# Performance work log

Measured on AMD Instinct MI355X. Metric: run time of the kernel, lower is better.

Reference implementation:

```python
import jax, jax.numpy as jnp
import numpy as np

IN_DIM = 128
OUT_DIM = 128
H = 8
HD = OUT_DIM // H  # 16
EPS = 1e-5
NEG = -1e30


def setup_inputs() -> dict:
    key = jax.random.key(0)
    ks = jax.random.split(key, 10)
    B, N = 8, 1024
    h = jax.random.normal(ks[0], (B, N, IN_DIM), dtype=jnp.float32)
    adj_mask = jax.random.randint(ks[1], (B, N, N), 0, 2, dtype=jnp.int32)
    s = 1.0 / np.sqrt(IN_DIM)
    W = jax.random.normal(ks[2], (H, IN_DIM, HD), dtype=jnp.float32) * s
    a = jax.random.normal(ks[3], (H, 2 * HD), dtype=jnp.float32) * (1.0 / np.sqrt(2 * HD))
    ln1_g = jnp.ones((OUT_DIM,), jnp.float32)
    ln1_b = jnp.zeros((OUT_DIM,), jnp.float32)
    w1 = jax.random.normal(ks[4], (OUT_DIM, 2 * OUT_DIM), dtype=jnp.float32) * (1.0 / np.sqrt(OUT_DIM))
    b1 = jnp.zeros((2 * OUT_DIM,), jnp.float32)
    w2 = jax.random.normal(ks[5], (2 * OUT_DIM, OUT_DIM), dtype=jnp.float32) * (1.0 / np.sqrt(2 * OUT_DIM))
    b2 = jnp.zeros((OUT_DIM,), jnp.float32)
    ln2_g = jnp.ones((OUT_DIM,), jnp.float32)
    ln2_b = jnp.zeros((OUT_DIM,), jnp.float32)
    return dict(h=h, adj_mask=adj_mask, W=W, a=a, ln1_g=ln1_g, ln1_b=ln1_b,
                w1=w1, b1=b1, w2=w2, b2=b2, ln2_g=ln2_g, ln2_b=ln2_b)


def _layernorm(x, g, b):
    mu = jnp.mean(x, axis=-1, keepdims=True)
    var = jnp.mean(jnp.square(x - mu), axis=-1, keepdims=True)
    return (x - mu) * jax.lax.rsqrt(var + EPS) * g + b


def reference(h, adj_mask, W, a, ln1_g, ln1_b, w1, b1, w2, b2, ln2_g, ln2_b):
    B, N, _ = h.shape
    # Per-head projection: (B,H,N,HD)
    Wh = jnp.einsum('bni,hid->bhnd', h, W)
    # a.[Wh_i, Wh_j] = a_src.Wh_i + a_dst.Wh_j (decompose concat-score)
    a_src, a_dst = a[:, :HD], a[:, HD:]
    s_i = jnp.einsum('bhnd,hd->bhn', Wh, a_src)  # source term
    s_j = jnp.einsum('bhnd,hd->bhn', Wh, a_dst)  # target term
    e = s_i[:, :, :, None] + s_j[:, :, None, :]  # (B,H,N,N)
    e = jnp.where(e >= 0, e, 0.2 * e)            # LeakyReLU(0.2)
    mask = (adj_mask != 0)[:, None, :, :]        # (B,1,N,N)
    e = jnp.where(mask, e, NEG)
    alpha = jax.nn.softmax(e, axis=-1)
    # rows with no neighbors -> NaN in torch softmax -> zeroed; replicate
    row_valid = jnp.any(mask, axis=-1, keepdims=True)  # (B,1,N,1)
    alpha = jnp.where(row_valid, alpha, 0.0)
    # dropout in eval mode = identity
    h_heads = jnp.einsum('bhnm,bhmd->bhnd', alpha, Wh)
    h_cat = h_heads.transpose(0, 2, 1, 3).reshape(B, N, H * HD)
    # residual (in_dim == out_dim here)
    h_cat = _layernorm(h_cat + h, ln1_g, ln1_b)
    ffn = jnp.maximum(h_cat @ w1 + b1, 0.0) @ w2 + b2
    return _layernorm(h_cat + ffn, ln2_g, ln2_b)
```

## Files before the change

kernel.cpp:

```cpp
#include <hip/hip_runtime.h>
#include <hip/hip_bf16.h>

#define IN_DIM 128
#define OUT_DIM 128
#define NHEAD 8
#define HD 16
#define BB 8
#define NN 1024
#define LOG2E 1.44269504f

typedef unsigned long long u64;
typedef float f32x4 __attribute__((ext_vector_type(4)));
typedef short bf16x8 __attribute__((ext_vector_type(8)));


__global__ __launch_bounds__(256) void k_pack(const int* __restrict__ adj,
                                              unsigned* __restrict__ bits_t,
                                              const float* __restrict__ w1,
                                              const float* __restrict__ w2,
                                              unsigned short* __restrict__ w1T,
                                              unsigned short* __restrict__ w2T) {
    __shared__ float tile[32][33];
    int t = threadIdx.x;
    if (blockIdx.x < 2048) {
        int lane = t & 63;
        int wave_id = blockIdx.x * 4 + (t >> 6);
        int b = wave_id >> 10, i = wave_id & 1023;
        const int4* rowp = (const int4*)(adj + ((size_t)(b * 1024 + i)) * 1024);
        int4 v0 = rowp[lane];
        int4 v1 = rowp[64 + lane];
        int4 v2 = rowp[128 + lane];
        int4 v3 = rowp[192 + lane];
        u64 B0x = __ballot(v0.x != 0), B0y = __ballot(v0.y != 0), B0z = __ballot(v0.z != 0), B0w = __ballot(v0.w != 0);
        u64 B1x = __ballot(v1.x != 0), B1y = __ballot(v1.y != 0), B1z = __ballot(v1.z != 0), B1w = __ballot(v1.w != 0);
        u64 B2x = __ballot(v2.x != 0), B2y = __ballot(v2.y != 0), B2z = __ballot(v2.z != 0), B2w = __ballot(v2.w != 0);
        u64 B3x = __ballot(v3.x != 0), B3y = __ballot(v3.y != 0), B3z = __ballot(v3.z != 0), B3w = __ballot(v3.w != 0);
        if (lane == 0) {
            unsigned* dst = bits_t + (size_t)b * 32 * 1024 + i;
#define STW(ch, c, B) \
            dst[((ch) * 8 + (c) * 2 + 0) * 1024] = (unsigned)(B); \
            dst[((ch) * 8 + (c) * 2 + 1) * 1024] = (unsigned)((B) >> 32);
            STW(0, 0, B0x) STW(0, 1, B0y) STW(0, 2, B0z) STW(0, 3, B0w)
            STW(1, 0, B1x) STW(1, 1, B1y) STW(1, 2, B1z) STW(1, 3, B1w)
            STW(2, 0, B2x) STW(2, 1, B2y) STW(2, 2, B2z) STW(2, 3, B2w)
            STW(3, 0, B3x) STW(3, 1, B3y) STW(3, 2, B3z) STW(3, 3, B3w)
#undef STW
        }
    } else {
        int blk = blockIdx.x - 2048;
        const float* src; unsigned short* dst; int R, C;
        if (blk < 32) { src = w1; dst = w1T; R = 128; C = 256; }
        else          { src = w2; dst = w2T; R = 256; C = 128; blk -= 32; }
        int tpr = C >> 5;
        int tr = blk / tpr, tc = blk - tr * tpr;
        int r0 = tr << 5, c0 = tc << 5;
        int lr = t >> 5, lc = t & 31;
#pragma unroll
        for (int p = 0; p < 4; ++p)
            tile[lr + p * 8][lc] = src[(size_t)(r0 + lr + p * 8) * C + c0 + lc];
        __syncthreads();
#pragma unroll
        for (int p = 0; p < 4; ++p) {
            __hip_bfloat16 bv = __float2bfloat16(tile[lc][lr + p * 8]);
            dst[(size_t)(c0 + lr + p * 8) * R + r0 + lc] = *(unsigned short*)&bv;
        }
    }
}

__global__ __launch_bounds__(256) void k_wh(
    const float* __restrict__ hin, const float* __restrict__ W,
    const float* __restrict__ a,
    unsigned short* __restrict__ whT, float* __restrict__ si_g,
    float* __restrict__ sj_g)
{
    extern __shared__ float smem[];
    float* h_s  = smem;
    float* wt_s = smem + 32 * 132;
    int t = threadIdx.x;
    int blk = blockIdx.x;
    int b = blk >> 5;
    int ntile = blk & 31;
    const float* hrow = hin + ((size_t)b * NN + ntile * 32) * IN_DIM;

#pragma unroll
    for (int it = 0; it < 4; ++it) {
        int g = t + 256 * it;
        int row = g >> 5, c4 = g & 31;
        float4 v = ((const float4*)hrow)[g];
        *(float4*)&h_s[row * 132 + c4 * 4] = v;
    }
    for (int g = t; g < (NHEAD * IN_DIM * HD) / 4; g += 256) {
        int hh = g >> 9;
        int rem = g & 511;
        int i = rem >> 2, d4 = rem & 3;
        float4 v = ((const float4*)W)[g];
        wt_s[(hh * 16 + d4 * 4 + 0) * 132 + i] = v.x;
        wt_s[(hh * 16 + d4 * 4 + 1) * 132 + i] = v.y;
        wt_s[(hh * 16 + d4 * 4 + 2) * 132 + i] = v.z;
        wt_s[(hh * 16 + d4 * 4 + 3) * 132 + i] = v.w;
    }
    __syncthreads();

    int d4 = t & 3;
    int hq = (t >> 2) & 7;
    int ngrp = t >> 5;
    float acc[4][4];
#pragma unroll
    for (int q = 0; q < 4; ++q)
#pragma unroll
        for (int dd = 0; dd < 4; ++dd) acc[q][dd] = 0.f;

    for (int i4 = 0; i4 < 32; ++i4) {
        float4 wr[4], hv[4];
#pragma unroll
        for (int dd = 0; dd < 4; ++dd)
            wr[dd] = *(const float4*)&wt_s[(hq * 16 + d4 * 4 + dd) * 132 + i4 * 4];
#pragma unroll
        for (int q = 0; q < 4; ++q)
            hv[q] = *(const float4*)&h_s[(ngrp * 4 + q) * 132 + i4 * 4];
#pragma unroll
        for (int q = 0; q < 4; ++q)
#pragma unroll
            for (int dd = 0; dd < 4; ++dd)
                acc[q][dd] += hv[q].x * wr[dd].x + hv[q].y * wr[dd].y +
                              hv[q].z * wr[dd].z + hv[q].w * wr[dd].w;
    }

    int bh = b * NHEAD + hq;
    int rowbase = ntile * 32 + ngrp * 4;
    int p0 = ((rowbase >> 8) << 8) | ((rowbase >> 2) & 63);

    float asrc[4], adst[4];
#pragma unroll
    for (int dd = 0; dd < 4; ++dd) {
        asrc[dd] = a[hq * 32 + d4 * 4 + dd];
        adst[dd] = a[hq * 32 + 16 + d4 * 4 + dd];
    }
#pragma unroll
    for (int q = 0; q < 4; ++q) {
        float psi = acc[q][0] * asrc[0] + acc[q][1] * asrc[1] + acc[q][2] * asrc[2] + acc[q][3] * asrc[3];
        float psj = acc[q][0] * adst[0] + acc[q][1] * adst[1] + acc[q][2] * adst[2] + acc[q][3] * adst[3];
        psi += __shfl_xor(psi, 1); psi += __shfl_xor(psi, 2);
        psj += __shfl_xor(psj, 1); psj += __shfl_xor(psj, 2);
        if (d4 == 0) {
            si_g[(size_t)bh * NN + rowbase + q] = psi * LOG2E;
            sj_g[(size_t)bh * NN + p0 + q * 64] = psj * LOG2E;
        }
    }

#pragma unroll
    for (int dd = 0; dd < 4; ++dd) {
        unsigned u0, u1;
        asm("v_cvt_pk_bf16_f32 %0, %1, %2" : "=v"(u0) : "v"(acc[0][dd]), "v"(acc[1][dd]));
        asm("v_cvt_pk_bf16_f32 %0, %1, %2" : "=v"(u1) : "v"(acc[2][dd]), "v"(acc[3][dd]));
        size_t basei = (size_t)(bh * 16 + d4 * 4 + dd) * 1024 + p0;
        whT[basei]       = (unsigned short)(u0 & 0xffff);
        whT[basei + 64]  = (unsigned short)(u0 >> 16);
        whT[basei + 128] = (unsigned short)(u1 & 0xffff);
        whT[basei + 192] = (unsigned short)(u1 >> 16);
    }
}

__global__ __launch_bounds__(512, 3) void k_attn(
    const unsigned short* __restrict__ whT,
    const unsigned* __restrict__ bits_t,
    const float* __restrict__ si_g, const float* __restrict__ sj_g,
    float* __restrict__ hh)
{
    __shared__ __align__(16) unsigned short whT_s[16 * 1032];
    __shared__ __align__(16) float ejp_s[NN];
    __shared__ __align__(16) float ejn_s[NN];
    int t = threadIdx.x;
    int blk = blockIdx.x;
    int part = blk & 7;
    int bh = blk >> 3;
    int hq = bh & 7, b = bh >> 3;
    int blkrow = part * 128;

    {
        const uint4* src = (const uint4*)(whT + (size_t)bh * 16 * 1024);
#pragma unroll
        for (int it = 0; it < 4; ++it) {
            int g = t + 512 * it;
            int d = g >> 7, c8 = g & 127;
            uint4 v = src[g];
            *(uint4*)&whT_s[d * 1032 + c8 * 8] = v;
        }
#pragma unroll
        for (int jt = 0; jt < 2; ++jt) {
            int j = t + jt * 512;
            float sjv = sj_g[(size_t)bh * NN + j];
            float ep, en;
            asm("v_exp_f32 %0, %1" : "=v"(ep) : "v"(sjv));
            asm("v_exp_f32 %0, %1" : "=v"(en) : "v"(0.2f * sjv));
            ejp_s[j] = ep;
            ejn_s[j] = en;
        }
    }
    __syncthreads();

    int wv = t >> 6, lane = t & 63;
    int lo16 = lane & 15, g = lane >> 4;
    int row = blkrow + wv * 16 + lo16;
    float siL = si_g[(size_t)bh * NN + row];
    float esip, esin;
    asm("v_exp_f32 %0, %1" : "=v"(esip) : "v"(siL));
    asm("v_exp_f32 %0, %1" : "=v"(esin) : "v"(0.2f * siL));
    const unsigned* mcol = bits_t + (size_t)b * 32 * 1024 + row;

    const unsigned short* wbase = &whT_s[lo16 * 1032 + g * 8];
    const float* pbase = &ejp_s[g * 8];
    const float* nbase = &ejn_s[g * 8];

    f32x4 acc = {0.f, 0.f, 0.f, 0.f};
    float lsA = 0.f, lsB = 0.f;
    unsigned m = mcol[0];
#pragma unroll 4
    for (int kt = 0; kt < 32; ++kt) {
        unsigned m_next = (kt < 31) ? mcol[(size_t)(kt + 1) * 1024] : 0u;
        bf16x8 bfrag = *(const bf16x8*)&wbase[kt * 32];
        float4 pa = *(const float4*)&pbase[kt * 32];
        float4 pb = *(const float4*)&pbase[kt * 32 + 4];
        float4 na = *(const float4*)&nbase[kt * 32];
        float4 nb = *(const float4*)&nbase[kt * 32 + 4];
        unsigned mm = m >> (g * 8);
        float q0 = fmaxf(esip * pa.x, esin * na.x); q0 = (mm & 1u)   ? q0 : 0.f;
        float q1 = fmaxf(esip * pa.y, esin * na.y); q1 = (mm & 2u)   ? q1 : 0.f;
        float q2 = fmaxf(esip * pa.z, esin * na.z); q2 = (mm & 4u)   ? q2 : 0.f;
        float q3 = fmaxf(esip * pa.w, esin * na.w); q3 = (mm & 8u)   ? q3 : 0.f;
        float q4 = fmaxf(esip * pb.x, esin * nb.x); q4 = (mm & 16u)  ? q4 : 0.f;
        float q5 = fmaxf(esip * pb.y, esin * nb.y); q5 = (mm & 32u)  ? q5 : 0.f;
        float q6 = fmaxf(esip * pb.z, esin * nb.z); q6 = (mm & 64u)  ? q6 : 0.f;
        float q7 = fmaxf(esip * pb.w, esin * nb.w); q7 = (mm & 128u) ? q7 : 0.f;
        lsA += (q0 + q2) + (q4 + q6);
        lsB += (q1 + q3) + (q5 + q7);
        union { bf16x8 v; __hip_bfloat16 h[8]; } af;
        af.h[0] = __float2bfloat16(q0);
        af.h[1] = __float2bfloat16(q1);
        af.h[2] = __float2bfloat16(q2);
        af.h[3] = __float2bfloat16(q3);
        af.h[4] = __float2bfloat16(q4);
        af.h[5] = __float2bfloat16(q5);
        af.h[6] = __float2bfloat16(q6);
        af.h[7] = __float2bfloat16(q7);
        acc = __builtin_amdgcn_mfma_f32_16x16x32_bf16(af.v, bfrag, acc, 0, 0, 0);
        m = m_next;
    }

    float lsum = lsA + lsB;
    lsum += __shfl_xor(lsum, 16);
    lsum += __shfl_xor(lsum, 32);

    float* obase = hh + ((size_t)b * NN + blkrow + wv * 16) * OUT_DIM + hq * HD + lo16;
#pragma unroll
    for (int q = 0; q < 4; ++q) {
        float ls = __shfl(lsum, 4 * g + q);
        float r = (ls > 0.f) ? 1.0f / ls : 0.f;
        obase[(size_t)(4 * g + q) * OUT_DIM] = acc[q] * r;
    }
}

__global__ __launch_bounds__(512, 1) void k_ffn(const float* __restrict__ hhs,
                                                const float* __restrict__ hin,
                                                const float* __restrict__ g1,
                                                const float* __restrict__ bt1,
                                                const unsigned short* __restrict__ w1T,
                                                const float* __restrict__ bb1,
                                                const unsigned short* __restrict__ w2T,
                                                const float* __restrict__ bb2,
                                                const float* __restrict__ g2,
                                                const float* __restrict__ bt2,
                                                float* __restrict__ out) {
    __shared__ float xc_f[32][128];
    __shared__ float y_f[32][132];
    __shared__ __align__(16) unsigned short xc_bf[32 * 128];
    __shared__ __align__(16) unsigned short hid_bf[32 * 256];

    int t = threadIdx.x;
    int R0 = blockIdx.x * 32;
    int wv = t >> 6, lane = t & 63;
    int lo = lane & 15, g = lane >> 4;

    bf16x8 b1f[2][4];
#pragma unroll
    for (int jt = 0; jt < 2; ++jt) {
        int n = (wv * 2 + jt) * 16 + lo;
#pragma unroll
        for (int kt = 0; kt < 4; ++kt)
            b1f[jt][kt] = *(const bf16x8*)&w1T[(size_t)n * 128 + kt * 32 + g * 8];
    }
    bf16x8 b2f[8];
    {
        int n = wv * 16 + lo;
#pragma unroll
        for (int kt = 0; kt < 8; ++kt)
            b2f[kt] = *(const bf16x8*)&w2T[(size_t)n * 256 + kt * 32 + g * 8];
    }
    float b1v[2];
    b1v[0] = bb1[(wv * 2 + 0) * 16 + lo];
    b1v[1] = bb1[(wv * 2 + 1) * 16 + lo];
    float b2v = bb2[wv * 16 + lo];

    {
        int r = t >> 4, c = t & 15;
        size_t row = (size_t)(R0 + r) * 128;
        float4 ha = *(const float4*)&hhs[row + c * 8];
        float4 hb = *(const float4*)&hhs[row + c * 8 + 4];
        float4 ia = *(const float4*)&hin[row + c * 8];
        float4 ib = *(const float4*)&hin[row + c * 8 + 4];
        float x[8] = {ha.x + ia.x, ha.y + ia.y, ha.z + ia.z, ha.w + ia.w,
                      hb.x + ib.x, hb.y + ib.y, hb.z + ib.z, hb.w + ib.w};
        float s = 0.f, s2 = 0.f;
#pragma unroll
        for (int j = 0; j < 8; ++j) { s += x[j]; s2 += x[j] * x[j]; }
#pragma unroll
        for (int off = 8; off > 0; off >>= 1) {
            s += __shfl_xor(s, off);
            s2 += __shfl_xor(s2, off);
        }
        float mu = s * (1.f / 128.f);
        float var = s2 * (1.f / 128.f) - mu * mu;
        float rs = rsqrtf(var + 1e-5f);
        float4 ga = *(const float4*)&g1[c * 8], gb = *(const float4*)&g1[c * 8 + 4];
        float4 ba = *(const float4*)&bt1[c * 8], bb = *(const float4*)&bt1[c * 8 + 4];
        float gg[8] = {ga.x, ga.y, ga.z, ga.w, gb.x, gb.y, gb.z, gb.w};
        float bbv[8] = {ba.x, ba.y, ba.z, ba.w, bb.x, bb.y, bb.z, bb.w};
        float xo[8];
#pragma unroll
        for (int j = 0; j < 8; ++j) xo[j] = (x[j] - mu) * rs * gg[j] + bbv[j];
        *(float4*)&xc_f[r][c * 8]     = make_float4(xo[0], xo[1], xo[2], xo[3]);
        *(float4*)&xc_f[r][c * 8 + 4] = make_float4(xo[4], xo[5], xo[6], xo[7]);
        union { uint4 v; unsigned u[4]; } pk;
#pragma unroll
        for (int q = 0; q < 4; ++q)
            asm("v_cvt_pk_bf16_f32 %0, %1, %2" : "=v"(pk.u[q]) : "v"(xo[2 * q]), "v"(xo[2 * q + 1]));
        int byte = (r * 256 + c * 16) ^ ((r & 7) << 4);
        *(uint4*)((char*)xc_bf + byte) = pk.v;
    }
    __syncthreads();

    {
        bf16x8 af[2][4];
#pragma unroll
        for (int mt = 0; mt < 2; ++mt) {
            int m = mt * 16 + lo;
#pragma unroll
            for (int kt = 0; kt < 4; ++kt) {
                int byte = (m * 256 + kt * 64 + g * 16) ^ ((m & 7) << 4);
                af[mt][kt] = *(const bf16x8*)((const char*)xc_bf + byte);
            }
        }
#pragma unroll
        for (int mt = 0; mt < 2; ++mt)
#pragma unroll
            for (int jt = 0; jt < 2; ++jt) {
                f32x4 acc = {0.f, 0.f, 0.f, 0.f};
#pragma unroll
                for (int kt = 0; kt < 4; ++kt)
                    acc = __builtin_amdgcn_mfma_f32_16x16x32_bf16(af[mt][kt], b1f[jt][kt], acc, 0, 0, 0);
                int n = (wv * 2 + jt) * 16 + lo;
#pragma unroll
                for (int q = 0; q < 4; ++q) {
                    float hv = fmaxf(acc[q] + b1v[jt], 0.f);
                    int m = mt * 16 + 4 * g + q;
                    int byte = (m * 512 + n * 2) ^ ((m & 7) << 4);
                    __hip_bfloat16 bv = __float2bfloat16(hv);
                    *(unsigned short*)((char*)hid_bf + byte) = *(unsigned short*)&bv;
                }
            }
    }
    __syncthreads();

    {
        f32x4 acc2[2] = {{0.f, 0.f, 0.f, 0.f}, {0.f, 0.f, 0.f, 0.f}};
#pragma unroll
        for (int mt = 0; mt < 2; ++mt) {
            int m = mt * 16 + lo;
#pragma unroll
            for (int kt = 0; kt < 8; ++kt) {
                int byte = (m * 512 + kt * 64 + g * 16) ^ ((m & 7) << 4);
                bf16x8 a = *(const bf16x8*)((const char*)hid_bf + byte);
                acc2[mt] = __builtin_amdgcn_mfma_f32_16x16x32_bf16(a, b2f[kt], acc2[mt], 0, 0, 0);
            }
        }
        int n = wv * 16 + lo;
#pragma unroll
        for (int mt = 0; mt < 2; ++mt)
#pragma unroll
            for (int q = 0; q < 4; ++q)
                y_f[mt * 16 + 4 * g + q][n] = acc2[mt][q] + b2v;
    }
    __syncthreads();

    {
        int r = t >> 4, c = t & 15;
        float xv[8];
        float s = 0.f, s2 = 0.f;
#pragma unroll
        for (int j = 0; j < 8; ++j) {
            float v = xc_f[r][c * 8 + j] + y_f[r][c * 8 + j];
            xv[j] = v; s += v; s2 += v * v;
        }
#pragma unroll
        for (int off = 8; off > 0; off >>= 1) {
            s += __shfl_xor(s, off);
            s2 += __shfl_xor(s2, off);
        }
        float mu = s * (1.f / 128.f);
        float var = s2 * (1.f / 128.f) - mu * mu;
        float rs = rsqrtf(var + 1e-5f);
        float4 ga = *(const float4*)&g2[c * 8], gb = *(const float4*)&g2[c * 8 + 4];
        float4 ba = *(const float4*)&bt2[c * 8], bb = *(const float4*)&bt2[c * 8 + 4];
        float o[8] = {(xv[0] - mu) * rs * ga.x + ba.x, (xv[1] - mu) * rs * ga.y + ba.y,
                      (xv[2] - mu) * rs * ga.z + ba.z, (xv[3] - mu) * rs * ga.w + ba.w,
                      (xv[4] - mu) * rs * gb.x + bb.x, (xv[5] - mu) * rs * gb.y + bb.y,
                      (xv[6] - mu) * rs * gb.z + bb.z, (xv[7] - mu) * rs * gb.w + bb.w};
        size_t row = (size_t)(R0 + r) * 128;
        *(float4*)&out[row + c * 8]     = make_float4(o[0], o[1], o[2], o[3]);
        *(float4*)&out[row + c * 8 + 4] = make_float4(o[4], o[5], o[6], o[7]);
    }
}

extern "C" void kernel_launch(void* const* d_in, const int* in_sizes, int n_in,
                              void* d_out, int out_size, void* d_ws, size_t ws_size,
                              hipStream_t stream) {
    const float* hin  = (const float*)d_in[0];
    const int*   adj  = (const int*)d_in[1];
    const float* W    = (const float*)d_in[2];
    const float* a    = (const float*)d_in[3];
    const float* ln1g = (const float*)d_in[4];
    const float* ln1b = (const float*)d_in[5];
    const float* w1   = (const float*)d_in[6];
    const float* b1   = (const float*)d_in[7];
    const float* w2   = (const float*)d_in[8];
    const float* b2   = (const float*)d_in[9];
    const float* ln2g = (const float*)d_in[10];
    const float* ln2b = (const float*)d_in[11];
    float* out = (float*)d_out;

    unsigned* bits_t    = (unsigned*)d_ws;
    unsigned short* whT = (unsigned short*)((char*)d_ws + (1u << 20));
    float* si_g         = (float*)((char*)d_ws + (3u << 20));
    float* sj_g         = (float*)((char*)d_ws + (3u << 20) + (256u << 10));
    float* hh           = (float*)((char*)d_ws + (3u << 20) + (512u << 10));
    unsigned short* w1T = (unsigned short*)((char*)d_ws + (7u << 20) + (512u << 10));
    unsigned short* w2T = (unsigned short*)((char*)d_ws + (7u << 20) + (512u << 10) + 65536);

    k_pack<<<2112, 256, 0, stream>>>(adj, bits_t, w1, w2, w1T, w2T);
    k_wh<<<BB * 32, 256, (32 * 132 + 128 * 132) * sizeof(float), stream>>>(hin, W, a, whT, si_g, sj_g);
    k_attn<<<BB * NHEAD * 8, 512, 0, stream>>>(whT, bits_t, si_g, sj_g, hh);
    k_ffn<<<BB * NN / 32, 512, 0, stream>>>(hh, hin, ln1g, ln1b, w1T, b1, w2T, b2, ln2g, ln2b, out);
}
```

Before: 56.39 us.

## Fuse all four stages into one cooperative persistent kernel with grid syncs

Replaces the four separate launches (mask packing, projection, attention, FFN) with a single cooperative kernel of 256 blocks that run each stage in turn, separated by grid-wide syncs. Work is redistributed to fit the fixed grid: each block now handles 256 attention rows over two passes and packs four mask rows per wave. The aim is to remove launch gaps and per-kernel tail effects. In exchange, parallelism is capped at one 512-thread block per CU-sized slot, and grid.sync adds its own barrier cost.

New measurement: 217.2 us. 3.85x slower.

```diff
diff --git a/kernel.cpp b/kernel.cpp
--- a/kernel.cpp
+++ b/kernel.cpp
@@ -1,5 +1,8 @@
 #include <hip/hip_runtime.h>
+#include <hip/hip_cooperative_groups.h>
 #include <hip/hip_bf16.h>
+
+namespace cg = cooperative_groups;
 
 #define IN_DIM 128
 #define OUT_DIM 128
@@ -14,410 +17,403 @@
 typedef short bf16x8 __attribute__((ext_vector_type(8)));
 
 
-__global__ __launch_bounds__(256) void k_pack(const int* __restrict__ adj,
-                                              unsigned* __restrict__ bits_t,
-                                              const float* __restrict__ w1,
-                                              const float* __restrict__ w2,
-                                              unsigned short* __restrict__ w1T,
-                                              unsigned short* __restrict__ w2T) {
-    __shared__ float tile[32][33];
+__global__ __launch_bounds__(512, 1) void k_fused(
+    const float* __restrict__ hin, const int* __restrict__ adj,
+    const float* __restrict__ W, const float* __restrict__ a,
+    const float* __restrict__ g1, const float* __restrict__ bt1,
+    const float* __restrict__ w1, const float* __restrict__ b1v_,
+    const float* __restrict__ w2, const float* __restrict__ b2v_,
+    const float* __restrict__ g2, const float* __restrict__ bt2,
+    unsigned* __restrict__ bits_t, unsigned short* __restrict__ whT,
+    float* __restrict__ si_g, float* __restrict__ sj_g,
+    float* __restrict__ hh, unsigned short* __restrict__ w1T,
+    unsigned short* __restrict__ w2T, float* __restrict__ out)
+{
+    __shared__ __align__(16) char smem_raw[84480];
     int t = threadIdx.x;
-    if (blockIdx.x < 2048) {
+    int blk = blockIdx.x;
+    cg::grid_group grid = cg::this_grid();
+
+    {
         int lane = t & 63;
-        int wave_id = blockIdx.x * 4 + (t >> 6);
-        int b = wave_id >> 10, i = wave_id & 1023;
-        const int4* rowp = (const int4*)(adj + ((size_t)(b * 1024 + i)) * 1024);
-        int4 v0 = rowp[lane];
-        int4 v1 = rowp[64 + lane];
-        int4 v2 = rowp[128 + lane];
-        int4 v3 = rowp[192 + lane];
-        u64 B0x = __ballot(v0.x != 0), B0y = __ballot(v0.y != 0), B0z = __ballot(v0.z != 0), B0w = __ballot(v0.w != 0);
-        u64 B1x = __ballot(v1.x != 0), B1y = __ballot(v1.y != 0), B1z = __ballot(v1.z != 0), B1w = __ballot(v1.w != 0);
-        u64 B2x = __ballot(v2.x != 0), B2y = __ballot(v2.y != 0), B2z = __ballot(v2.z != 0), B2w = __ballot(v2.w != 0);
-        u64 B3x = __ballot(v3.x != 0), B3y = __ballot(v3.y != 0), B3z = __ballot(v3.z != 0), B3w = __ballot(v3.w != 0);
-        if (lane == 0) {
-            unsigned* dst = bits_t + (size_t)b * 32 * 1024 + i;
+        int wave_id = blk * 8 + (t >> 6);
+#pragma unroll 1
+        for (int u = 0; u < 4; ++u) {
+            int r = wave_id + u * 2048;
+            int b = r >> 10, i = r & 1023;
+            const int4* rowp = (const int4*)(adj + ((size_t)(b * 1024 + i)) * 1024);
+            int4 v0 = rowp[lane];
+            int4 v1 = rowp[64 + lane];
+            int4 v2 = rowp[128 + lane];
+            int4 v3 = rowp[192 + lane];
+            u64 B0x = __ballot(v0.x != 0), B0y = __ballot(v0.y != 0), B0z = __ballot(v0.z != 0), B0w = __ballot(v0.w != 0);
+            u64 B1x = __ballot(v1.x != 0), B1y = __ballot(v1.y != 0), B1z = __ballot(v1.z != 0), B1w = __ballot(v1.w != 0);
+            u64 B2x = __ballot(v2.x != 0), B2y = __ballot(v2.y != 0), B2z = __ballot(v2.z != 0), B2w = __ballot(v2.w != 0);
+            u64 B3x = __ballot(v3.x != 0), B3y = __ballot(v3.y != 0), B3z = __ballot(v3.z != 0), B3w = __ballot(v3.w != 0);
+            if (lane == 0) {
+                unsigned* dst = bits_t + (size_t)b * 32 * 1024 + i;
 #define STW(ch, c, B) \
-            dst[((ch) * 8 + (c) * 2 + 0) * 1024] = (unsigned)(B); \
-            dst[((ch) * 8 + (c) * 2 + 1) * 1024] = (unsigned)((B) >> 32);
-            STW(0, 0, B0x) STW(0, 1, B0y) STW(0, 2, B0z) STW(0, 3, B0w)
-            STW(1, 0, B1x) STW(1, 1, B1y) STW(1, 2, B1z) STW(1, 3, B1w)
-            STW(2, 0, B2x) STW(2, 1, B2y) STW(2, 2, B2z) STW(2, 3, B2w)
-            STW(3, 0, B3x) STW(3, 1, B3y) STW(3, 2, B3z) STW(3, 3, B3w)
+                dst[((ch) * 8 + (c) * 2 + 0) * 1024] = (unsigned)(B); \
+                dst[((ch) * 8 + (c) * 2 + 1) * 1024] = (unsigned)((B) >> 32);
+                STW(0, 0, B0x) STW(0, 1, B0y) STW(0, 2, B0z) STW(0, 3, B0w)
+                STW(1, 0, B1x) STW(1, 1, B1y) STW(1, 2, B1z) STW(1, 3, B1w)
+                STW(2, 0, B2x) STW(2, 1, B2y) STW(2, 2, B2z) STW(2, 3, B2w)
+                STW(3, 0, B3x) STW(3, 1, B3y) STW(3, 2, B3z) STW(3, 3, B3w)
 #undef STW
-        }
-    } else {
-        int blk = blockIdx.x - 2048;
+            }
+        }
+    }
+    {
+        float* h_s  = (float*)smem_raw;
+        float* wt_s = h_s + 32 * 132;
+        int b = blk >> 5, ntile = blk & 31;
+        const float* hrow = hin + ((size_t)b * NN + ntile * 32) * IN_DIM;
+        for (int g4 = t; g4 < 1024; g4 += 512) {
+            int row = g4 >> 5, c4 = g4 & 31;
+            float4 v = ((const float4*)hrow)[g4];
+            *(float4*)&h_s[row * 132 + c4 * 4] = v;
+        }
+        for (int g4 = t; g4 < (NHEAD * IN_DIM * HD) / 4; g4 += 512) {
+            int hh_ = g4 >> 9;
+            int rem = g4 & 511;
+            int i = rem >> 2, d4 = rem & 3;
+            float4 v = ((const float4*)W)[g4];
+            wt_s[(hh_ * 16 + d4 * 4 + 0) * 132 + i] = v.x;
+            wt_s[(hh_ * 16 + d4 * 4 + 1) * 132 + i] = v.y;
+            wt_s[(hh_ * 16 + d4 * 4 + 2) * 132 + i] = v.z;
+            wt_s[(hh_ * 16 + d4 * 4 + 3) * 132 + i] = v.w;
+        }
+        __syncthreads();
+
+        if (t < 256) {
+            int d4 = t & 3;
+            int hq = (t >> 2) & 7;
+            int ngrp = t >> 5;
+            float acc[4][4];
+#pragma unroll
+            for (int q = 0; q < 4; ++q)
+#pragma unroll
+                for (int dd = 0; dd < 4; ++dd) acc[q][dd] = 0.f;
+
+            for (int i4 = 0; i4 < 32; ++i4) {
+                float4 wr[4], hv[4];
+#pragma unroll
+                for (int dd = 0; dd < 4; ++dd)
+                    wr[dd] = *(const float4*)&wt_s[(hq * 16 + d4 * 4 + dd) * 132 + i4 * 4];
+#pragma unroll
+                for (int q = 0; q < 4; ++q)
+                    hv[q] = *(const float4*)&h_s[(ngrp * 4 + q) * 132 + i4 * 4];
+#pragma unroll
+                for (int q = 0; q < 4; ++q)
+#pragma unroll
+                    for (int dd = 0; dd < 4; ++dd)
+                        acc[q][dd] += hv[q].x * wr[dd].x + hv[q].y * wr[dd].y +
+                                      hv[q].z * wr[dd].z + hv[q].w * wr[dd].w;
+            }
+
+            int bh = b * NHEAD + hq;
+            int rowbase = ntile * 32 + ngrp * 4;
+            int p0 = ((rowbase >> 8) << 8) | ((rowbase >> 2) & 63);
+
+            float asrc[4], adst[4];
+#pragma unroll
+            for (int dd = 0; dd < 4; ++dd) {
+                asrc[dd] = a[hq * 32 + d4 * 4 + dd];
+                adst[dd] = a[hq * 32 + 16 + d4 * 4 + dd];
+            }
+#pragma unroll
+            for (int q = 0; q < 4; ++q) {
+                float psi = acc[q][0] * asrc[0] + acc[q][1] * asrc[1] + acc[q][2] * asrc[2] + acc[q][3] * asrc[3];
+                float psj = acc[q][0] * adst[0] + acc[q][1] * adst[1] + acc[q][2] * adst[2] + acc[q][3] * adst[3];
+                psi += __shfl_xor(psi, 1); psi += __shfl_xor(psi, 2);
+                psj += __shfl_xor(psj, 1); psj += __shfl_xor(psj, 2);
+                if (d4 == 0) {
+                    si_g[(size_t)bh * NN + rowbase + q] = psi * LOG2E;
+                    sj_g[(size_t)bh * NN + p0 + q * 64] = psj * LOG2E;
+                }
+            }
+#pragma unroll
+            for (int dd = 0; dd < 4; ++dd) {
+                unsigned u0, u1;
+                asm("v_cvt_pk_bf16_f32 %0, %1, %2" : "=v"(u0) : "v"(acc[0][dd]), "v"(acc[1][dd]));
+                asm("v_cvt_pk_bf16_f32 %0, %1, %2" : "=v"(u1) : "v"(acc[2][dd]), "v"(acc[3][dd]));
+                size_t basei = (size_t)(bh * 16 + d4 * 4 + dd) * 1024 + p0;
+                whT[basei]       = (unsigned short)(u0 & 0xffff);
+                whT[basei + 64]  = (unsigned short)(u0 >> 16);
+                whT[basei + 128] = (unsigned short)(u1 & 0xffff);
+                whT[basei + 192] = (unsigned short)(u1 >> 16);
+            }
+        }
+    }
+    if (blk < 64) {
+        __syncthreads();
+        float* tile = (float*)smem_raw;
+        int bb = blk;
         const float* src; unsigned short* dst; int R, C;
-        if (blk < 32) { src = w1; dst = w1T; R = 128; C = 256; }
-        else          { src = w2; dst = w2T; R = 256; C = 128; blk -= 32; }
+        if (bb < 32) { src = w1; dst = w1T; R = 128; C = 256; }
+        else         { src = w2; dst = w2T; R = 256; C = 128; bb -= 32; }
         int tpr = C >> 5;
-        int tr = blk / tpr, tc = blk - tr * tpr;
+        int tr = bb / tpr, tc = bb - tr * tpr;
         int r0 = tr << 5, c0 = tc << 5;
         int lr = t >> 5, lc = t & 31;
 #pragma unroll
-        for (int p = 0; p < 4; ++p)
-            tile[lr + p * 8][lc] = src[(size_t)(r0 + lr + p * 8) * C + c0 + lc];
-        __syncthreads();
-#pragma unroll
-        for (int p = 0; p < 4; ++p) {
-            __hip_bfloat16 bv = __float2bfloat16(tile[lc][lr + p * 8]);
-            dst[(size_t)(c0 + lr + p * 8) * R + r0 + lc] = *(unsigned short*)&bv;
+        for (int p = 0; p < 2; ++p)
+            tile[(lr + p * 16) * 33 + lc] = src[(size_t)(r0 + lr + p * 16) * C + c0 + lc];
+        __syncthreads();
+#pragma unroll
+        for (int p = 0; p < 2; ++p) {
+            __hip_bfloat16 bv = __float2bfloat16(tile[lc * 33 + lr + p * 16]);
+            dst[(size_t)(c0 + lr + p * 16) * R + r0 + lc] = *(unsigned short*)&bv;
         }
     }
-}
-
-__global__ __launch_bounds__(256) void k_wh(
-    const float* __restrict__ hin, const float* __restrict__ W,
-    const float* __restrict__ a,
-    unsigned short* __restrict__ whT, float* __restrict__ si_g,
-    float* __restrict__ sj_g)
-{
-    extern __shared__ float smem[];
-    float* h_s  = smem;
-    float* wt_s = smem + 32 * 132;
-    int t = threadIdx.x;
-    int blk = blockIdx.x;
-    int b = blk >> 5;
-    int ntile = blk & 31;
-    const float* hrow = hin + ((size_t)b * NN + ntile * 32) * IN_DIM;
-
-#pragma unroll
-    for (int it = 0; it < 4; ++it) {
-        int g = t + 256 * it;
-        int row = g >> 5, c4 = g & 31;
-        float4 v = ((const float4*)hrow)[g];
-        *(float4*)&h_s[row * 132 + c4 * 4] = v;
+    __threadfence();
+    grid.sync();
+
+    {
+        unsigned short* whT_s = (unsigned short*)smem_raw;
+        float* ejp_s = (float*)(smem_raw + 16 * 1032 * 2);
+        float* ejn_s = ejp_s + NN;
+        int bh = blk >> 2;
+        int q4 = blk & 3;
+        int hq = bh & 7, b = bh >> 3;
+
+        {
+            const uint4* src = (const uint4*)(whT + (size_t)bh * 16 * 1024);
+#pragma unroll
+            for (int it = 0; it < 4; ++it) {
+                int g4 = t + 512 * it;
+                int d = g4 >> 7, c8 = g4 & 127;
+                uint4 v = src[g4];
+                *(uint4*)&whT_s[d * 1032 + c8 * 8] = v;
+            }
+#pragma unroll
+            for (int jt = 0; jt < 2; ++jt) {
+                int j = t + jt * 512;
+                float sjv = sj_g[(size_t)bh * NN + j];
+                float ep, en;
+                asm("v_exp_f32 %0, %1" : "=v"(ep) : "v"(sjv));
+                asm("v_exp_f32 %0, %1" : "=v"(en) : "v"(0.2f * sjv));
+                ejp_s[j] = ep;
+                ejn_s[j] = en;
+            }
+        }
+        __syncthreads();
+
+        int wv = t >> 6, lane = t & 63;
+        int lo16 = lane & 15, g = lane >> 4;
+        const unsigned short* wbase = &whT_s[lo16 * 1032 + g * 8];
+        const float* pbase = &ejp_s[g * 8];
+        const float* nbase = &ejn_s[g * 8];
+
+#pragma unroll 1
+        for (int pr = 0; pr < 2; ++pr) {
+            int blkrow = q4 * 256 + pr * 128;
+            int row = blkrow + wv * 16 + lo16;
+            float siL = si_g[(size_t)bh * NN + row];
+            float esip, esin;
+            asm("v_exp_f32 %0, %1" : "=v"(esip) : "v"(siL));
+            asm("v_exp_f32 %0, %1" : "=v"(esin) : "v"(0.2f * siL));
+            const unsigned* mcol = bits_t + (size_t)b * 32 * 1024 + row;
+
+            f32x4 acc = {0.f, 0.f, 0.f, 0.f};
+            float lsA = 0.f, lsB = 0.f;
+            unsigned m = mcol[0];
+#pragma unroll 4
+            for (int kt = 0; kt < 32; ++kt) {
+                unsigned m_next = (kt < 31) ? mcol[(size_t)(kt + 1) * 1024] : 0u;
+                bf16x8 bfrag = *(const bf16x8*)&wbase[kt * 32];
+                float4 pa = *(const float4*)&pbase[kt * 32];
+                float4 pb = *(const float4*)&pbase[kt * 32 + 4];
+                float4 na = *(const float4*)&nbase[kt * 32];
+                float4 nb = *(const float4*)&nbase[kt * 32 + 4];
+                unsigned mm = m >> (g * 8);
+                float q0 = fmaxf(esip * pa.x, esin * na.x); q0 = (mm & 1u)   ? q0 : 0.f;
+                float q1 = fmaxf(esip * pa.y, esin * na.y); q1 = (mm & 2u)   ? q1 : 0.f;
+                float q2 = fmaxf(esip * pa.z, esin * na.z); q2 = (mm & 4u)   ? q2 : 0.f;
+                float q3 = fmaxf(esip * pa.w, esin * na.w); q3 = (mm & 8u)   ? q3 : 0.f;
+                float q4v = fmaxf(esip * pb.x, esin * nb.x); q4v = (mm & 16u)  ? q4v : 0.f;
+                float q5 = fmaxf(esip * pb.y, esin * nb.y); q5 = (mm & 32u)  ? q5 : 0.f;
+                float q6 = fmaxf(esip * pb.z, esin * nb.z); q6 = (mm & 64u)  ? q6 : 0.f;
+                float q7 = fmaxf(esip * pb.w, esin * nb.w); q7 = (mm & 128u) ? q7 : 0.f;
+                lsA += (q0 + q2) + (q4v + q6);
+                lsB += (q1 + q3) + (q5 + q7);
+                union { bf16x8 v; __hip_bfloat16 h[8]; } af;
+                af.h[0] = __float2bfloat16(q0);
+                af.h[1] = __float2bfloat16(q1);
+                af.h[2] = __float2bfloat16(q2);
+                af.h[3] = __float2bfloat16(q3);
+                af.h[4] = __float2bfloat16(q4v);
+                af.h[5] = __float2bfloat16(q5);
+                af.h[6] = __float2bfloat16(q6);
+                af.h[7] = __float2bfloat16(q7);
+                acc = __builtin_amdgcn_mfma_f32_16x16x32_bf16(af.v, bfrag, acc, 0, 0, 0);
+                m = m_next;
+            }
+
+            float lsum = lsA + lsB;
+            lsum += __shfl_xor(lsum, 16);
+            lsum += __shfl_xor(lsum, 32);
+
+            float* obase = hh + ((size_t)b * NN + blkrow + wv * 16) * OUT_DIM + hq * HD + lo16;
+#pragma unroll
+            for (int q = 0; q < 4; ++q) {
+                float ls = __shfl(lsum, 4 * g + q);
+                float r = (ls > 0.f) ? 1.0f / ls : 0.f;
+                obase[(size_t)(4 * g + q) * OUT_DIM] = acc[q] * r;
+            }
+        }
     }
-    for (int g = t; g < (NHEAD * IN_DIM * HD) / 4; g += 256) {
-        int hh = g >> 9;
-        int rem = g & 511;
-        int i = rem >> 2, d4 = rem & 3;
-        float4 v = ((const float4*)W)[g];
-        wt_s[(hh * 16 + d4 * 4 + 0) * 132 + i] = v.x;
-        wt_s[(hh * 16 + d4 * 4 + 1) * 132 + i] = v.y;
-        wt_s[(hh * 16 + d4 * 4 + 2) * 132 + i] = v.z;
-        wt_s[(hh * 16 + d4 * 4 + 3) * 132 + i] = v.w;
-    }
-    __syncthreads();
-
-    int d4 = t & 3;
-    int hq = (t >> 2) & 7;
-    int ngrp = t >> 5;
-    float acc[4][4];
-#pragma unroll
-    for (int q = 0; q < 4; ++q)
-#pragma unroll
-        for (int dd = 0; dd < 4; ++dd) acc[q][dd] = 0.f;
-
-    for (int i4 = 0; i4 < 32; ++i4) {
-        float4 wr[4], hv[4];
-#pragma unroll
-        for (int dd = 0; dd < 4; ++dd)
-            wr[dd] = *(const float4*)&wt_s[(hq * 16 + d4 * 4 + dd) * 132 + i4 * 4];
-#pragma unroll
-        for (int q = 0; q < 4; ++q)
-            hv[q] = *(const float4*)&h_s[(ngrp * 4 + q) * 132 + i4 * 4];
-#pragma unroll
-        for (int q = 0; q < 4; ++q)
-#pragma unroll
-            for (int dd = 0; dd < 4; ++dd)
-                acc[q][dd] += hv[q].x * wr[dd].x + hv[q].y * wr[dd].y +
-                              hv[q].z * wr[dd].z + hv[q].w * wr[dd].w;
-    }
-
-    int bh = b * NHEAD + hq;
-    int rowbase = ntile * 32 + ngrp * 4;
-    int p0 = ((rowbase >> 8) << 8) | ((rowbase >> 2) & 63);
-
-    float asrc[4], adst[4];
-#pragma unroll
-    for (int dd = 0; dd < 4; ++dd) {
-        asrc[dd] = a[hq * 32 + d4 * 4 + dd];
-        adst[dd] = a[hq * 32 + 16 + d4 * 4 + dd];
-    }
-#pragma unroll
-    for (int q = 0; q < 4; ++q) {
-        float psi = acc[q][0] * asrc[0] + acc[q][1] * asrc[1] + acc[q][2] * asrc[2] + acc[q][3] * asrc[3];
-        float psj = acc[q][0] * adst[0] + acc[q][1] * adst[1] + acc[q][2] * adst[2] + acc[q][3] * adst[3];
-        psi += __shfl_xor(psi, 1); psi += __shfl_xor(psi, 2);
-        psj += __shfl_xor(psj, 1); psj += __shfl_xor(psj, 2);
-        if (d4 == 0) {
-            si_g[(size_t)bh * NN + rowbase + q] = psi * LOG2E;
-            sj_g[(size_t)bh * NN + p0 + q * 64] = psj * LOG2E;
-        }
-    }
-
-#pragma unroll
-    for (int dd = 0; dd < 4; ++dd) {
-        unsigned u0, u1;
-        asm("v_cvt_pk_bf16_f32 %0, %1, %2" : "=v"(u0) : "v"(acc[0][dd]), "v"(acc[1][dd]));
-        asm("v_cvt_pk_bf16_f32 %0, %1, %2" : "=v"(u1) : "v"(acc[2][dd]), "v"(acc[3][dd]));
-        size_t basei = (size_t)(bh * 16 + d4 * 4 + dd) * 1024 + p0;
-        whT[basei]       = (unsigned short)(u0 & 0xffff);
-        whT[basei + 64]  = (unsigned short)(u0 >> 16);
-        whT[basei + 128] = (unsigned short)(u1 & 0xffff);
-        whT[basei + 192] = (unsigned short)(u1 >> 16);
-    }
-}
-
-__global__ __launch_bounds__(512, 3) void k_attn(
-    const unsigned short* __restrict__ whT,
-    const unsigned* __restrict__ bits_t,
-    const float* __restrict__ si_g, const float* __restrict__ sj_g,
-    float* __restrict__ hh)
-{
-    __shared__ __align__(16) unsigned short whT_s[16 * 1032];
-    __shared__ __align__(16) float ejp_s[NN];
-    __shared__ __align__(16) float ejn_s[NN];
-    int t = threadIdx.x;
-    int blk = blockIdx.x;
-    int part = blk & 7;
-    int bh = blk >> 3;
-    int hq = bh & 7, b = bh >> 3;
-    int blkrow = part * 128;
+    __threadfence();
+    grid.sync();
 
     {
-        const uint4* src = (const uint4*)(whT + (size_t)bh * 16 * 1024);
-#pragma unroll
-        for (int it = 0; it < 4; ++it) {
-            int g = t + 512 * it;
-            int d = g >> 7, c8 = g & 127;
-            uint4 v = src[g];
-            *(uint4*)&whT_s[d * 1032 + c8 * 8] = v;
-        }
+        float* xc_f = (float*)smem_raw;
+        float* y_f  = (float*)(smem_raw + 16384);
+        unsigned short* xc_bf  = (unsigned short*)(smem_raw + 33280);
+        unsigned short* hid_bf = (unsigned short*)(smem_raw + 41472);
+
+        int R0 = blk * 32;
+        int wv = t >> 6, lane = t & 63;
+        int lo = lane & 15, g = lane >> 4;
+
+        bf16x8 b1f[2][4];
 #pragma unroll
         for (int jt = 0; jt < 2; ++jt) {
-            int j = t + jt * 512;
-            float sjv = sj_g[(size_t)bh * NN + j];
-            float ep, en;
-            asm("v_exp_f32 %0, %1" : "=v"(ep) : "v"(sjv));
-            asm("v_exp_f32 %0, %1" : "=v"(en) : "v"(0.2f * sjv));
-            ejp_s[j] = ep;
-            ejn_s[j] = en;
-        }
-    }
-    __syncthreads();
-
-    int wv = t >> 6, lane = t & 63;
-    int lo16 = lane & 15, g = lane >> 4;
-    int row = blkrow + wv * 16 + lo16;
-    float siL = si_g[(size_t)bh * NN + row];
-    float esip, esin;
-    asm("v_exp_f32 %0, %1" : "=v"(esip) : "v"(siL));
-    asm("v_exp_f32 %0, %1" : "=v"(esin) : "v"(0.2f * siL));
-    const unsigned* mcol = bits_t + (size_t)b * 32 * 1024 + row;
-
-    const unsigned short* wbase = &whT_s[lo16 * 1032 + g * 8];
-    const float* pbase = &ejp_s[g * 8];
-    const float* nbase = &ejn_s[g * 8];
-
-    f32x4 acc = {0.f, 0.f, 0.f, 0.f};
-    float lsA = 0.f, lsB = 0.f;
-    unsigned m = mcol[0];
-#pragma unroll 4
-    for (int kt = 0; kt < 32; ++kt) {
-        unsigned m_next = (kt < 31) ? mcol[(size_t)(kt + 1) * 1024] : 0u;
-        bf16x8 bfrag = *(const bf16x8*)&wbase[kt * 32];
-        float4 pa = *(const float4*)&pbase[kt * 32];
-        float4 pb = *(const float4*)&pbase[kt * 32 + 4];
-        float4 na = *(const float4*)&nbase[kt * 32];
-        float4 nb = *(const float4*)&nbase[kt * 32 + 4];
-        unsigned mm = m >> (g * 8);
-        float q0 = fmaxf(esip * pa.x, esin * na.x); q0 = (mm & 1u)   ? q0 : 0.f;
-        float q1 = fmaxf(esip * pa.y, esin * na.y); q1 = (mm & 2u)   ? q1 : 0.f;
-        float q2 = fmaxf(esip * pa.z, esin * na.z); q2 = (mm & 4u)   ? q2 : 0.f;
-        float q3 = fmaxf(esip * pa.w, esin * na.w); q3 = (mm & 8u)   ? q3 : 0.f;
-        float q4 = fmaxf(esip * pb.x, esin * nb.x); q4 = (mm & 16u)  ? q4 : 0.f;
-        float q5 = fmaxf(esip * pb.y, esin * nb.y); q5 = (mm & 32u)  ? q5 : 0.f;
-        float q6 = fmaxf(esip * pb.z, esin * nb.z); q6 = (mm & 64u)  ? q6 : 0.f;
-        float q7 = fmaxf(esip * pb.w, esin * nb.w); q7 = (mm & 128u) ? q7 : 0.f;
-        lsA += (q0 + q2) + (q4 + q6);
-        lsB += (q1 + q3) + (q5 + q7);
-        union { bf16x8 v; __hip_bfloat16 h[8]; } af;
-        af.h[0] = __float2bfloat16(q0);
-        af.h[1] = __float2bfloat16(q1);
-        af.h[2] = __float2bfloat16(q2);
-        af.h[3] = __float2bfloat16(q3);
-        af.h[4] = __float2bfloat16(q4);
-        af.h[5] = __float2bfloat16(q5);
-        af.h[6] = __float2bfloat16(q6);
-        af.h[7] = __float2bfloat16(q7);
-        acc = __builtin_amdgcn_mfma_f32_16x16x32_bf16(af.v, bfrag, acc, 0, 0, 0);
-        m = m_next;
-    }
-
-    float lsum = lsA + lsB;
-    lsum += __shfl_xor(lsum, 16);
-    lsum += __shfl_xor(lsum, 32);
-
-    float* obase = hh + ((size_t)b * NN + blkrow + wv * 16) * OUT_DIM + hq * HD + lo16;
-#pragma unroll
-    for (int q = 0; q < 4; ++q) {
-        float ls = __shfl(lsum, 4 * g + q);
-        float r = (ls > 0.f) ? 1.0f / ls : 0.f;
-        obase[(size_t)(4 * g + q) * OUT_DIM] = acc[q] * r;
-    }
-}
-
-__global__ __launch_bounds__(512, 1) void k_ffn(const float* __restrict__ hhs,
-                                                const float* __restrict__ hin,
-                                                const float* __restrict__ g1,
-                                                const float* __restrict__ bt1,
-                                                const unsigned short* __restrict__ w1T,
-                                                const float* __restrict__ bb1,
-                                                const unsigned short* __restrict__ w2T,
-                                                const float* __restrict__ bb2,
-                                                const float* __restrict__ g2,
-                                                const float* __restrict__ bt2,
-                                                float* __restrict__ out) {
-    __shared__ float xc_f[32][128];
-    __shared__ float y_f[32][132];
-    __shared__ __align__(16) unsigned short xc_bf[32 * 128];
-    __shared__ __align__(16) unsigned short hid_bf[32 * 256];
-
-    int t = threadIdx.x;
-    int R0 = blockIdx.x * 32;
-    int wv = t >> 6, lane = t & 63;
-    int lo = lane & 15, g = lane >> 4;
-
-    bf16x8 b1f[2][4];
-#pragma unroll
-    for (int jt = 0; jt < 2; ++jt) {
-        int n = (wv * 2 + jt) * 16 + lo;
-#pragma unroll
-        for (int kt = 0; kt < 4; ++kt)
-            b1f[jt][kt] = *(const bf16x8*)&w1T[(size_t)n * 128 + kt * 32 + g * 8];
-    }
-    bf16x8 b2f[8];
-    {
-        int n = wv * 16 + lo;
-#pragma unroll
-        for (int kt = 0; kt < 8; ++kt)
-            b2f[kt] = *(const bf16x8*)&w2T[(size_t)n * 256 + kt * 32 + g * 8];
-    }
-    float b1v[2];
-    b1v[0] = bb1[(wv * 2 + 0) * 16 + lo];
-    b1v[1] = bb1[(wv * 2 + 1) * 16 + lo];
-    float b2v = bb2[wv * 16 + lo];
-
-    {
-        int r = t >> 4, c = t & 15;
-        size_t row = (size_t)(R0 + r) * 128;
-        float4 ha = *(const float4*)&hhs[row + c * 8];
-        float4 hb = *(const float4*)&hhs[row + c * 8 + 4];
-        float4 ia = *(const float4*)&hin[row + c * 8];
-        float4 ib = *(const float4*)&hin[row + c * 8 + 4];
-        float x[8] = {ha.x + ia.x, ha.y + ia.y, ha.z + ia.z, ha.w + ia.w,
-                      hb.x + ib.x, hb.y + ib.y, hb.z + ib.z, hb.w + ib.w};
-        float s = 0.f, s2 = 0.f;
-#pragma unroll
-        for (int j = 0; j < 8; ++j) { s += x[j]; s2 += x[j] * x[j]; }
-#pragma unroll
-        for (int off = 8; off > 0; off >>= 1) {
-            s += __shfl_xor(s, off);
-            s2 += __shfl_xor(s2, off);
-        }
-        float mu = s * (1.f / 128.f);
-        float var = s2 * (1.f / 128.f) - mu * mu;
-        float rs = rsqrtf(var + 1e-5f);
-        float4 ga = *(const float4*)&g1[c * 8], gb = *(const float4*)&g1[c * 8 + 4];
-        float4 ba = *(const float4*)&bt1[c * 8], bb = *(const float4*)&bt1[c * 8 + 4];
-        float gg[8] = {ga.x, ga.y, ga.z, ga.w, gb.x, gb.y, gb.z, gb.w};
-        float bbv[8] = {ba.x, ba.y, ba.z, ba.w, bb.x, bb.y, bb.z, bb.w};
-        float xo[8];
-#pragma unroll
-        for (int j = 0; j < 8; ++j) xo[j] = (x[j] - mu) * rs * gg[j] + bbv[j];
-        *(float4*)&xc_f[r][c * 8]     = make_float4(xo[0], xo[1], xo[2], xo[3]);
-        *(float4*)&xc_f[r][c * 8 + 4] = make_float4(xo[4], xo[5], xo[6], xo[7]);
-        union { uint4 v; unsigned u[4]; } pk;
-#pragma unroll
-        for (int q = 0; q < 4; ++q)
-            asm("v_cvt_pk_bf16_f32 %0, %1, %2" : "=v"(pk.u[q]) : "v"(xo[2 * q]), "v"(xo[2 * q + 1]));
-        int byte = (r * 256 + c * 16) ^ ((r & 7) << 4);
-        *(uint4*)((char*)xc_bf + byte) = pk.v;
-    }
-    __syncthreads();
-
-    {
-        bf16x8 af[2][4];
-#pragma unroll
-        for (int mt = 0; mt < 2; ++mt) {
-            int m = mt * 16 + lo;
-#pragma unroll
-            for (int kt = 0; kt < 4; ++kt) {
-                int byte = (m * 256 + kt * 64 + g * 16) ^ ((m & 7) << 4);
-                af[mt][kt] = *(const bf16x8*)((const char*)xc_bf + byte);
-            }
-        }
-#pragma unroll
-        for (int mt = 0; mt < 2; ++mt)
-#pragma unroll
-            for (int jt = 0; jt < 2; ++jt) {
-                f32x4 acc = {0.f, 0.f, 0.f, 0.f};
-#pragma unroll
-                for (int kt = 0; kt < 4; ++kt)
-                    acc = __builtin_amdgcn_mfma_f32_16x16x32_bf16(af[mt][kt], b1f[jt][kt], acc, 0, 0, 0);
-                int n = (wv * 2 + jt) * 16 + lo;
-#pragma unroll
-                for (int q = 0; q < 4; ++q) {
-                    float hv = fmaxf(acc[q] + b1v[jt], 0.f);
-                    int m = mt * 16 + 4 * g + q;
-                    int byte = (m * 512 + n * 2) ^ ((m & 7) << 4);
-                    __hip_bfloat16 bv = __float2bfloat16(hv);
-                    *(unsigned short*)((char*)hid_bf + byte) = *(unsigned short*)&bv;
+            int n = (wv * 2 + jt) * 16 + lo;
+#pragma unroll
+            for (int kt = 0; kt < 4; ++kt)
+                b1f[jt][kt] = *(const bf16x8*)&w1T[(size_t)n * 128 + kt * 32 + g * 8];
+        }
+        bf16x8 b2f[8];
+        {
+            int n = wv * 16 + lo;
+#pragma unroll
+            for (int kt = 0; kt < 8; ++kt)
+                b2f[kt] = *(const bf16x8*)&w2T[(size_t)n * 256 + kt * 32 + g * 8];
+        }
+        float b1v[2];
+        b1v[0] = b1v_[(wv * 2 + 0) * 16 + lo];
+        b1v[1] = b1v_[(wv * 2 + 1) * 16 + lo];
+        float b2v = b2v_[wv * 16 + lo];
+
+        {
+            int r = t >> 4, c = t & 15;
+            size_t row = (size_t)(R0 + r) * 128;
+            float4 ha = *(const float4*)&hh[row + c * 8];
+            float4 hb = *(const float4*)&hh[row + c * 8 + 4];
+            float4 ia = *(const float4*)&hin[row + c * 8];
+            float4 ib = *(const float4*)&hin[row + c * 8 + 4];
+            float x[8] = {ha.x + ia.x, ha.y + ia.y, ha.z + ia.z, ha.w + ia.w,
+                          hb.x + ib.x, hb.y + ib.y, hb.z + ib.z, hb.w + ib.w};
+            float s = 0.f, s2 = 0.f;
+#pragma unroll
+            for (int j = 0; j < 8; ++j) { s += x[j]; s2 += x[j] * x[j]; }
+#pragma unroll
+            for (int off = 8; off > 0; off >>= 1) {
+                s += __shfl_xor(s, off);
+                s2 += __shfl_xor(s2, off);
+            }
+            float mu = s * (1.f / 128.f);
+            float var = s2 * (1.f / 128.f) - mu * mu;
+            float rs = rsqrtf(var + 1e-5f);
+            float4 ga = *(const float4*)&g1[c * 8], gb = *(const float4*)&g1[c * 8 + 4];
+            float4 ba = *(const float4*)&bt1[c * 8], bb = *(const float4*)&bt1[c * 8 + 4];
+            float gg[8] = {ga.x, ga.y, ga.z, ga.w, gb.x, gb.y, gb.z, gb.w};
+            float bbv[8] = {ba.x, ba.y, ba.z, ba.w, bb.x, bb.y, bb.z, bb.w};
+            float xo[8];
+#pragma unroll
+            for (int j = 0; j < 8; ++j) xo[j] = (x[j] - mu) * rs * gg[j] + bbv[j];
+            *(float4*)&xc_f[r * 128 + c * 8]     = make_float4(xo[0], xo[1], xo[2], xo[3]);
+            *(float4*)&xc_f[r * 128 + c * 8 + 4] = make_float4(xo[4], xo[5], xo[6], xo[7]);
+            union { uint4 v; unsigned u[4]; } pk;
+#pragma unroll
+            for (int q = 0; q < 4; ++q)
+                asm("v_cvt_pk_bf16_f32 %0, %1, %2" : "=v"(pk.u[q]) : "v"(xo[2 * q]), "v"(xo[2 * q + 1]));
+            int byte = (r * 256 + c * 16) ^ ((r & 7) << 4);
+            *(uint4*)((char*)xc_bf + byte) = pk.v;
+        }
+        __syncthreads();
+
+        {
+            bf16x8 af[2][4];
+#pragma unroll
+            for (int mt = 0; mt < 2; ++mt) {
+                int m = mt * 16 + lo;
+#pragma unroll
+                for (int kt = 0; kt < 4; ++kt) {
+                    int byte = (m * 256 + kt * 64 + g * 16) ^ ((m & 7) << 4);
+                    af[mt][kt] = *(const bf16x8*)((const char*)xc_bf + byte);
                 }
             }
-    }
-    __syncthreads();
-
-    {
-        f32x4 acc2[2] = {{0.f, 0.f, 0.f, 0.f}, {0.f, 0.f, 0.f, 0.f}};
-#pragma unroll
-        for (int mt = 0; mt < 2; ++mt) {
-            int m = mt * 16 + lo;
-#pragma unroll
-            for (int kt = 0; kt < 8; ++kt) {
-                int byte = (m * 512 + kt * 64 + g * 16) ^ ((m & 7) << 4);
-                bf16x8 a = *(const bf16x8*)((const char*)hid_bf + byte);
-                acc2[mt] = __builtin_amdgcn_mfma_f32_16x16x32_bf16(a, b2f[kt], acc2[mt], 0, 0, 0);
-            }
-        }
-        int n = wv * 16 + lo;
-#pragma unroll
-        for (int mt = 0; mt < 2; ++mt)
-#pragma unroll
-            for (int q = 0; q < 4; ++q)
-                y_f[mt * 16 + 4 * g + q][n] = acc2[mt][q] + b2v;
-    }
-    __syncthreads();
-
-    {
-        int r = t >> 4, c = t & 15;
-        float xv[8];
-        float s = 0.f, s2 = 0.f;
-#pragma unroll
-        for (int j = 0; j < 8; ++j) {
-            float v = xc_f[r][c * 8 + j] + y_f[r][c * 8 + j];
-            xv[j] = v; s += v; s2 += v * v;
-        }
-#pragma unroll
-        for (int off = 8; off > 0; off >>= 1) {
-            s += __shfl_xor(s, off);
-            s2 += __shfl_xor(s2, off);
-        }
-        float mu = s * (1.f / 128.f);
-        float var = s2 * (1.f / 128.f) - mu * mu;
-        float rs = rsqrtf(var + 1e-5f);
-        float4 ga = *(const float4*)&g2[c * 8], gb = *(const float4*)&g2[c * 8 + 4];
-        float4 ba = *(const float4*)&bt2[c * 8], bb = *(const float4*)&bt2[c * 8 + 4];
-        float o[8] = {(xv[0] - mu) * rs * ga.x + ba.x, (xv[1] - mu) * rs * ga.y + ba.y,
-                      (xv[2] - mu) * rs * ga.z + ba.z, (xv[3] - mu) * rs * ga.w + ba.w,
-                      (xv[4] - mu) * rs * gb.x + bb.x, (xv[5] - mu) * rs * gb.y + bb.y,
-                      (xv[6] - mu) * rs * gb.z + bb.z, (xv[7] - mu) * rs * gb.w + bb.w};
-        size_t row = (size_t)(R0 + r) * 128;
-        *(float4*)&out[row + c * 8]     = make_float4(o[0], o[1], o[2], o[3]);
-        *(float4*)&out[row + c * 8 + 4] = make_float4(o[4], o[5], o[6], o[7]);
+#pragma unroll
+            for (int mt = 0; mt < 2; ++mt)
+#pragma unroll
+                for (int jt = 0; jt < 2; ++jt) {
+                    f32x4 acc = {0.f, 0.f, 0.f, 0.f};
+#pragma unroll
+                    for (int kt = 0; kt < 4; ++kt)
+                        acc = __builtin_amdgcn_mfma_f32_16x16x32_bf16(af[mt][kt], b1f[jt][kt], acc, 0, 0, 0);
+                    int n = (wv * 2 + jt) * 16 + lo;
+#pragma unroll
+                    for (int q = 0; q < 4; ++q) {
+                        float hv = fmaxf(acc[q] + b1v[jt], 0.f);
+                        int m = mt * 16 + 4 * g + q;
+                        int byte = (m * 512 + n * 2) ^ ((m & 7) << 4);
+                        __hip_bfloat16 bv = __float2bfloat16(hv);
+                        *(unsigned short*)((char*)hid_bf + byte) = *(unsigned short*)&bv;
+                    }
+                }
+        }
+        __syncthreads();
+
+        {
+            f32x4 acc2[2] = {{0.f, 0.f, 0.f, 0.f}, {0.f, 0.f, 0.f, 0.f}};
+#pragma unroll
+            for (int mt = 0; mt < 2; ++mt) {
+                int m = mt * 16 + lo;
+#pragma unroll
+                for (int kt = 0; kt < 8; ++kt) {
+                    int byte = (m * 512 + kt * 64 + g * 16) ^ ((m & 7) << 4);
+                    bf16x8 a2 = *(const bf16x8*)((const char*)hid_bf + byte);
+                    acc2[mt] = __builtin_amdgcn_mfma_f32_16x16x32_bf16(a2, b2f[kt], acc2[mt], 0, 0, 0);
+                }
+            }
+            int n = wv * 16 + lo;
+#pragma unroll
+            for (int mt = 0; mt < 2; ++mt)
+#pragma unroll
+                for (int q = 0; q < 4; ++q)
+                    y_f[(mt * 16 + 4 * g + q) * 132 + n] = acc2[mt][q] + b2v;
+        }
+        __syncthreads();
+
+        {
+            int r = t >> 4, c = t & 15;
+            float xv[8];
+            float s = 0.f, s2 = 0.f;
+#pragma unroll
+            for (int j = 0; j < 8; ++j) {
+                float v = xc_f[r * 128 + c * 8 + j] + y_f[r * 132 + c * 8 + j];
+                xv[j] = v; s += v; s2 += v * v;
+            }
+#pragma unroll
+            for (int off = 8; off > 0; off >>= 1) {
+                s += __shfl_xor(s, off);
+                s2 += __shfl_xor(s2, off);
+            }
+            float mu = s * (1.f / 128.f);
+            float var = s2 * (1.f / 128.f) - mu * mu;
+            float rs = rsqrtf(var + 1e-5f);
+            float4 ga = *(const float4*)&g2[c * 8], gb = *(const float4*)&g2[c * 8 + 4];
+            float4 ba = *(const float4*)&bt2[c * 8], bb = *(const float4*)&bt2[c * 8 + 4];
+            float o[8] = {(xv[0] - mu) * rs * ga.x + ba.x, (xv[1] - mu) * rs * ga.y + ba.y,
+                          (xv[2] - mu) * rs * ga.z + ba.z, (xv[3] - mu) * rs * ga.w + ba.w,
+                          (xv[4] - mu) * rs * gb.x + bb.x, (xv[5] - mu) * rs * gb.y + bb.y,
+                          (xv[6] - mu) * rs * gb.z + bb.z, (xv[7] - mu) * rs * gb.w + bb.w};
+            size_t row = (size_t)(R0 + r) * 128;
+            *(float4*)&out[row + c * 8]     = make_float4(o[0], o[1], o[2], o[3]);
+            *(float4*)&out[row + c * 8 + 4] = make_float4(o[4], o[5], o[6], o[7]);
+        }
     }
 }
 
@@ -446,8 +442,10 @@
     unsigned short* w1T = (unsigned short*)((char*)d_ws + (7u << 20) + (512u << 10));
     unsigned short* w2T = (unsigned short*)((char*)d_ws + (7u << 20) + (512u << 10) + 65536);
 
-    k_pack<<<2112, 256, 0, stream>>>(adj, bits_t, w1, w2, w1T, w2T);
-    k_wh<<<BB * 32, 256, (32 * 132 + 128 * 132) * sizeof(float), stream>>>(hin, W, a, whT, si_g, sj_g);
-    k_attn<<<BB * NHEAD * 8, 512, 0, stream>>>(whT, bits_t, si_g, sj_g, hh);
-    k_ffn<<<BB * NN / 32, 512, 0, stream>>>(hh, hin, ln1g, ln1b, w1T, b1, w2T, b2, ln2g, ln2b, out);
+    void* args[] = {(void*)&hin, (void*)&adj, (void*)&W, (void*)&a,
+                    (void*)&ln1g, (void*)&ln1b, (void*)&w1, (void*)&b1,
+                    (void*)&w2, (void*)&b2, (void*)&ln2g, (void*)&ln2b,
+                    (void*)&bits_t, (void*)&whT, (void*)&si_g, (void*)&sj_g,
+                    (void*)&hh, (void*)&w1T, (void*)&w2T, (void*)&out};
+    hipLaunchCooperativeKernel((void*)k_fused, dim3(256), dim3(512), args, 0, stream);
 }
```
